# Kernel optimization log

Hardware: AMD Instinct MI355X
Metric: run time of the kernel (lower is better)

## Reference

```python
import jax, jax.numpy as jnp
import numpy as np
import math

B, C, D_FEAT, D_TASK, HID = 1024, 256, 512, 512, 32


def setup_inputs() -> dict:
    key = jax.random.key(0)
    ks = jax.random.split(key, 10)
    def xavier(k, shape, gain):
        fan_out, fan_in = shape
        a = gain * math.sqrt(6.0 / (fan_in + fan_out))
        return jax.random.uniform(k, shape, jnp.float32, -a, a)
    return {
        "Q": jax.random.normal(ks[0], (B, D_TASK), jnp.float32),
        "features": jax.random.normal(ks[1], (B, C, D_FEAT), jnp.float32),
        "Wk_w": xavier(ks[2], (D_TASK, D_FEAT), 0.1),
        "Wk_b": jnp.zeros((D_TASK,), jnp.float32),
        "Wv_w": xavier(ks[3], (D_TASK, D_FEAT), 0.1),
        "Wv_b": jnp.zeros((D_TASK,), jnp.float32),
        "g1_w": xavier(ks[4], (HID, D_TASK + 1), 1.0),
        "g1_b": jax.random.uniform(ks[5], (HID,), jnp.float32, -1.0, 1.0) / math.sqrt(D_TASK + 1),
        "g2_w": xavier(ks[6], (1, HID), 0.1),
        "g2_b": jnp.zeros((1,), jnp.float32),
    }


def reference(Q, features, Wk_w, Wk_b, Wv_w, Wv_b, g1_w, g1_b, g2_w, g2_b):
    # K, V projections: [B, C, d_task]
    K = jnp.einsum('bcf,tf->bct', features, Wk_w) + Wk_b
    V = jnp.einsum('bcf,tf->bct', features, Wv_w) + Wv_b
    # single-query cross-attention
    scores = jnp.einsum('bt,bct->bc', Q, K) / math.sqrt(D_TASK)  # [B, C]
    weights = jax.nn.softmax(scores, axis=-1)
    feat_read = jnp.einsum('bc,bct->bt', weights, V)  # [B, d_task]
    # gate from (Q, feature scale)
    feat_scale = jnp.mean(jnp.abs(features), axis=(1, 2), keepdims=False)[:, None]  # [B, 1]
    h = jnp.concatenate([Q, feat_scale], axis=-1)  # [B, d_task+1]
    h = jax.nn.gelu(h @ g1_w.T + g1_b, approximate=False)
    gate = jax.nn.sigmoid(h @ g2_w.T + g2_b)  # [B, 1]
    return gate * feat_read, gate
```

## Files before the change

### kernel.cpp

```cpp
#include <hip/hip_runtime.h>
#include <math.h>

constexpr int B = 1024, C = 256, DF = 512, DT = 512, HID = 32;

__global__ __launch_bounds__(256) void qproj_kernel(const float* __restrict__ Q,
                                                    const float* __restrict__ Wk,
                                                    float* __restrict__ qtil) {
    __shared__ __align__(16) float qs[4][DT];
    const int tid = threadIdx.x;
    const int b0 = blockIdx.x * 4;
#pragma unroll
    for (int bb = 0; bb < 4; bb++) {
        qs[bb][tid]       = Q[(b0 + bb) * DT + tid];
        qs[bb][tid + 256] = Q[(b0 + bb) * DT + tid + 256];
    }
    __syncthreads();
    const int f0 = tid * 2;
    float acc0[4] = {0.f, 0.f, 0.f, 0.f};
    float acc1[4] = {0.f, 0.f, 0.f, 0.f};
    for (int t4 = 0; t4 < DT; t4 += 4) {
        float q[4][4];
#pragma unroll
        for (int bb = 0; bb < 4; bb++) {
            float4 qv = *(const float4*)&qs[bb][t4];
            q[bb][0] = qv.x; q[bb][1] = qv.y; q[bb][2] = qv.z; q[bb][3] = qv.w;
        }
#pragma unroll
        for (int k = 0; k < 4; k++) {
            float2 w = *(const float2*)(Wk + (size_t)(t4 + k) * DF + f0);
#pragma unroll
            for (int bb = 0; bb < 4; bb++) {
                acc0[bb] += q[bb][k] * w.x;
                acc1[bb] += q[bb][k] * w.y;
            }
        }
    }
#pragma unroll
    for (int bb = 0; bb < 4; bb++) {
        float2 o; o.x = acc0[bb]; o.y = acc1[bb];
        *(float2*)(qtil + (size_t)(b0 + bb) * DF + f0) = o;
    }
}

__global__ __launch_bounds__(256) void main_kernel(
    const float* __restrict__ Q, const float* __restrict__ feat,
    const float* __restrict__ qtil,
    const float* __restrict__ Wv, const float* __restrict__ Wvb,
    const float* __restrict__ g1w, const float* __restrict__ g1b,
    const float* __restrict__ g2w, const float* __restrict__ g2b,
    float* __restrict__ out0, float* __restrict__ out1) {

    __shared__ __align__(16) float s_q[DF];
    __shared__ __align__(16) float s_Q[DT];
    __shared__ __align__(16) float s_part[4][DF];
    __shared__ __align__(16) float s_r[DF];
    __shared__ __align__(16) float s_out[DT];
    __shared__ float s_m[4], s_l[4], s_abs[4];
    __shared__ float s_hp[HID][8];
    __shared__ float s_h[HID];
    __shared__ float s_gate;

    const int tid  = threadIdx.x;
    const int lane = tid & 63;
    const int wv   = tid >> 6;
    const int b    = blockIdx.x;

    s_q[tid]       = qtil[b * DF + tid];
    s_q[tid + 256] = qtil[b * DF + tid + 256];
    s_Q[tid]       = Q[b * DT + tid];
    s_Q[tid + 256] = Q[b * DT + tid + 256];
    __syncthreads();

    float qreg[8];
    {
        float4 a0 = *(const float4*)&s_q[lane * 8];
        float4 a1 = *(const float4*)&s_q[lane * 8 + 4];
        qreg[0] = a0.x; qreg[1] = a0.y; qreg[2] = a0.z; qreg[3] = a0.w;
        qreg[4] = a1.x; qreg[5] = a1.y; qreg[6] = a1.z; qreg[7] = a1.w;
    }

    const float* fb = feat + (size_t)b * C * DF;
    float r[8] = {0.f, 0.f, 0.f, 0.f, 0.f, 0.f, 0.f, 0.f};
    float m = -INFINITY, l = 0.f, sabs = 0.f;
    const float rs = 0.044194173824159216f;

    for (int c = wv * 64; c < wv * 64 + 64; c += 2) {
        const float* row0 = fb + (size_t)c * DF + lane * 8;
        const float* row1 = row0 + DF;
        float4 x0a = *(const float4*)row0;
        float4 x0b = *(const float4*)(row0 + 4);
        float4 x1a = *(const float4*)row1;
        float4 x1b = *(const float4*)(row1 + 4);
        float v0[8] = {x0a.x, x0a.y, x0a.z, x0a.w, x0b.x, x0b.y, x0b.z, x0b.w};
        float v1[8] = {x1a.x, x1a.y, x1a.z, x1a.w, x1b.x, x1b.y, x1b.z, x1b.w};
        float dot0 = 0.f, dot1 = 0.f;
#pragma unroll
        for (int j = 0; j < 8; j++) {
            dot0 += v0[j] * qreg[j];
            dot1 += v1[j] * qreg[j];
            sabs += fabsf(v0[j]) + fabsf(v1[j]);
        }
#pragma unroll
        for (int off = 1; off < 64; off <<= 1) {
            dot0 += __shfl_xor(dot0, off, 64);
            dot1 += __shfl_xor(dot1, off, 64);
        }
        float s0 = dot0 * rs, s1 = dot1 * rs;
        float m2 = fmaxf(fmaxf(m, s0), s1);
        float a  = __expf(m - m2);
        float p0 = __expf(s0 - m2);
        float p1 = __expf(s1 - m2);
        l = l * a + p0 + p1;
#pragma unroll
        for (int j = 0; j < 8; j++) r[j] = r[j] * a + p0 * v0[j] + p1 * v1[j];
        m = m2;
    }
#pragma unroll
    for (int off = 1; off < 64; off <<= 1) sabs += __shfl_xor(sabs, off, 64);
    if (lane == 0) { s_m[wv] = m; s_l[wv] = l; s_abs[wv] = sabs; }
    __syncthreads();

    float M = fmaxf(fmaxf(s_m[0], s_m[1]), fmaxf(s_m[2], s_m[3]));
    float L = s_l[0] * __expf(s_m[0] - M) + s_l[1] * __expf(s_m[1] - M) +
              s_l[2] * __expf(s_m[2] - M) + s_l[3] * __expf(s_m[3] - M);
    float msc = __expf(m - M);
#pragma unroll
    for (int j = 0; j < 8; j++) s_part[wv][lane * 8 + j] = r[j] * msc;
    float fscale = (s_abs[0] + s_abs[1] + s_abs[2] + s_abs[3]) * (1.0f / (float)(C * DF));
    __syncthreads();

    float invL = 1.0f / L;
#pragma unroll
    for (int k = 0; k < 2; k++) {
        int f = tid + 256 * k;
        s_r[f] = (s_part[0][f] + s_part[1][f] + s_part[2][f] + s_part[3][f]) * invL;
    }

    {
        int i = tid >> 3, g = tid & 7;
        const float* row = g1w + (size_t)i * (DT + 1);
        float part = 0.f;
        for (int t = g * 64; t < g * 64 + 64; ++t) part += row[t] * s_Q[t];
        if (g == 0) part += row[DT] * fscale;
        s_hp[i][g] = part;
    }
    __syncthreads();
    if (tid < HID) {
        float x = g1b[tid];
#pragma unroll
        for (int g = 0; g < 8; ++g) x += s_hp[tid][g];
        s_h[tid] = 0.5f * x * (1.0f + erff(x * 0.70710678118654752f));
    }
    __syncthreads();
    if (tid == 0) {
        float z = g2b[0];
        for (int i = 0; i < HID; ++i) z += s_h[i] * g2w[i];
        float gate = 1.0f / (1.0f + __expf(-z));
        s_gate = gate;
        out1[b] = gate;
    }
    __syncthreads();

    float gate = s_gate;
    float rr[8];
    {
        float4 a0 = *(const float4*)&s_r[lane * 8];
        float4 a1 = *(const float4*)&s_r[lane * 8 + 4];
        rr[0] = a0.x; rr[1] = a0.y; rr[2] = a0.z; rr[3] = a0.w;
        rr[4] = a1.x; rr[5] = a1.y; rr[6] = a1.z; rr[7] = a1.w;
    }
    for (int t = wv * 128; t < wv * 128 + 128; t += 2) {
        const float* w0p = Wv + (size_t)t * DF + lane * 8;
        const float* w1p = w0p + DF;
        float4 w0a = *(const float4*)w0p;
        float4 w0b = *(const float4*)(w0p + 4);
        float4 w1a = *(const float4*)w1p;
        float4 w1b = *(const float4*)(w1p + 4);
        float dot0 = w0a.x * rr[0] + w0a.y * rr[1] + w0a.z * rr[2] + w0a.w * rr[3]
                   + w0b.x * rr[4] + w0b.y * rr[5] + w0b.z * rr[6] + w0b.w * rr[7];
        float dot1 = w1a.x * rr[0] + w1a.y * rr[1] + w1a.z * rr[2] + w1a.w * rr[3]
                   + w1b.x * rr[4] + w1b.y * rr[5] + w1b.z * rr[6] + w1b.w * rr[7];
#pragma unroll
        for (int off = 1; off < 64; off <<= 1) {
            dot0 += __shfl_xor(dot0, off, 64);
            dot1 += __shfl_xor(dot1, off, 64);
        }
        if (lane == 0) {
            s_out[t]     = gate * (dot0 + Wvb[t]);
            s_out[t + 1] = gate * (dot1 + Wvb[t + 1]);
        }
    }
    __syncthreads();
    float2 o;
    o.x = s_out[2 * tid];
    o.y = s_out[2 * tid + 1];
    *(float2*)(out0 + (size_t)b * DT + 2 * tid) = o;
}

extern "C" void kernel_launch(void* const* d_in, const int* in_sizes, int n_in,
                              void* d_out, int out_size, void* d_ws, size_t ws_size,
                              hipStream_t stream) {
    const float* Q    = (const float*)d_in[0];
    const float* feat = (const float*)d_in[1];
    const float* Wk   = (const float*)d_in[2];
    const float* Wv   = (const float*)d_in[4];
    const float* Wvb  = (const float*)d_in[5];
    const float* g1w  = (const float*)d_in[6];
    const float* g1b  = (const float*)d_in[7];
    const float* g2w  = (const float*)d_in[8];
    const float* g2b  = (const float*)d_in[9];
    float* out0 = (float*)d_out;
    float* out1 = out0 + (size_t)B * DT;
    float* qtil = (float*)d_ws;

    hipLaunchKernelGGL(qproj_kernel, dim3(B / 4), dim3(256), 0, stream, Q, Wk, qtil);
    hipLaunchKernelGGL(main_kernel, dim3(B), dim3(256), 0, stream,
                       Q, feat, qtil, Wv, Wvb, g1w, g1b, g2w, g2b, out0, out1);
}
```

Before: 790.8 us.

## Split V projection into separate kernel batching four rows per Wv pass

```diff
diff --git a/kernel.cpp b/kernel.cpp
--- a/kernel.cpp
+++ b/kernel.cpp
@@ -45,20 +45,16 @@
 __global__ __launch_bounds__(256) void main_kernel(
     const float* __restrict__ Q, const float* __restrict__ feat,
     const float* __restrict__ qtil,
-    const float* __restrict__ Wv, const float* __restrict__ Wvb,
     const float* __restrict__ g1w, const float* __restrict__ g1b,
     const float* __restrict__ g2w, const float* __restrict__ g2b,
-    float* __restrict__ out0, float* __restrict__ out1) {
+    float* __restrict__ rg, float* __restrict__ out1) {
 
     __shared__ __align__(16) float s_q[DF];
     __shared__ __align__(16) float s_Q[DT];
     __shared__ __align__(16) float s_part[4][DF];
-    __shared__ __align__(16) float s_r[DF];
-    __shared__ __align__(16) float s_out[DT];
     __shared__ float s_m[4], s_l[4], s_abs[4];
     __shared__ float s_hp[HID][8];
     __shared__ float s_h[HID];
-    __shared__ float s_gate;
 
     const int tid  = threadIdx.x;
     const int lane = tid & 63;
@@ -133,7 +129,8 @@
 #pragma unroll
     for (int k = 0; k < 2; k++) {
         int f = tid + 256 * k;
-        s_r[f] = (s_part[0][f] + s_part[1][f] + s_part[2][f] + s_part[3][f]) * invL;
+        float val = (s_part[0][f] + s_part[1][f] + s_part[2][f] + s_part[3][f]) * invL;
+        rg[(size_t)b * DF + f] = val;
     }
 
     {
@@ -155,46 +152,82 @@
     if (tid == 0) {
         float z = g2b[0];
         for (int i = 0; i < HID; ++i) z += s_h[i] * g2w[i];
-        float gate = 1.0f / (1.0f + __expf(-z));
-        s_gate = gate;
-        out1[b] = gate;
-    }
-    __syncthreads();
-
-    float gate = s_gate;
-    float rr[8];
+        out1[b] = 1.0f / (1.0f + __expf(-z));
+    }
+}
+
+__global__ __launch_bounds__(512) void vproj_kernel(
+    const float* __restrict__ rg, const float* __restrict__ gates,
+    const float* __restrict__ Wv, const float* __restrict__ Wvb,
+    float* __restrict__ out0) {
+
+    __shared__ __align__(16) float s_r4[4][DF];
+    __shared__ __align__(16) float s_o[4][DT];
+
+    const int tid  = threadIdx.x;
+    const int lane = tid & 63;
+    const int wv   = tid >> 6;
+    const int b0   = blockIdx.x * 4;
+
     {
-        float4 a0 = *(const float4*)&s_r[lane * 8];
-        float4 a1 = *(const float4*)&s_r[lane * 8 + 4];
-        rr[0] = a0.x; rr[1] = a0.y; rr[2] = a0.z; rr[3] = a0.w;
-        rr[4] = a1.x; rr[5] = a1.y; rr[6] = a1.z; rr[7] = a1.w;
-    }
-    for (int t = wv * 128; t < wv * 128 + 128; t += 2) {
+        const float* src = rg + (size_t)b0 * DF;
+        float* dst = &s_r4[0][0];
+#pragma unroll
+        for (int k = 0; k < 4; k++) dst[tid + 512 * k] = src[tid + 512 * k];
+    }
+    __syncthreads();
+
+    float rr[4][8];
+#pragma unroll
+    for (int bb = 0; bb < 4; bb++) {
+        float4 a0 = *(const float4*)&s_r4[bb][lane * 8];
+        float4 a1 = *(const float4*)&s_r4[bb][lane * 8 + 4];
+        rr[bb][0] = a0.x; rr[bb][1] = a0.y; rr[bb][2] = a0.z; rr[bb][3] = a0.w;
+        rr[bb][4] = a1.x; rr[bb][5] = a1.y; rr[bb][6] = a1.z; rr[bb][7] = a1.w;
+    }
+    float g4[4];
+#pragma unroll
+    for (int bb = 0; bb < 4; bb++) g4[bb] = gates[b0 + bb];
+
+    for (int t = wv * 64; t < wv * 64 + 64; t += 2) {
         const float* w0p = Wv + (size_t)t * DF + lane * 8;
         const float* w1p = w0p + DF;
         float4 w0a = *(const float4*)w0p;
         float4 w0b = *(const float4*)(w0p + 4);
         float4 w1a = *(const float4*)w1p;
         float4 w1b = *(const float4*)(w1p + 4);
-        float dot0 = w0a.x * rr[0] + w0a.y * rr[1] + w0a.z * rr[2] + w0a.w * rr[3]
-                   + w0b.x * rr[4] + w0b.y * rr[5] + w0b.z * rr[6] + w0b.w * rr[7];
-        float dot1 = w1a.x * rr[0] + w1a.y * rr[1] + w1a.z * rr[2] + w1a.w * rr[3]
-                   + w1b.x * rr[4] + w1b.y * rr[5] + w1b.z * rr[6] + w1b.w * rr[7];
+        float w0[8] = {w0a.x, w0a.y, w0a.z, w0a.w, w0b.x, w0b.y, w0b.z, w0b.w};
+        float w1[8] = {w1a.x, w1a.y, w1a.z, w1a.w, w1b.x, w1b.y, w1b.z, w1b.w};
+        float d0[4], d1[4];
+#pragma unroll
+        for (int bb = 0; bb < 4; bb++) {
+            float a = 0.f, c = 0.f;
+#pragma unroll
+            for (int j = 0; j < 8; j++) {
+                a += w0[j] * rr[bb][j];
+                c += w1[j] * rr[bb][j];
+            }
+            d0[bb] = a; d1[bb] = c;
+        }
 #pragma unroll
         for (int off = 1; off < 64; off <<= 1) {
-            dot0 += __shfl_xor(dot0, off, 64);
-            dot1 += __shfl_xor(dot1, off, 64);
+#pragma unroll
+            for (int bb = 0; bb < 4; bb++) {
+                d0[bb] += __shfl_xor(d0[bb], off, 64);
+                d1[bb] += __shfl_xor(d1[bb], off, 64);
+            }
         }
         if (lane == 0) {
-            s_out[t]     = gate * (dot0 + Wvb[t]);
-            s_out[t + 1] = gate * (dot1 + Wvb[t + 1]);
-        }
-    }
-    __syncthreads();
-    float2 o;
-    o.x = s_out[2 * tid];
-    o.y = s_out[2 * tid + 1];
-    *(float2*)(out0 + (size_t)b * DT + 2 * tid) = o;
+            float vb0 = Wvb[t], vb1 = Wvb[t + 1];
+#pragma unroll
+            for (int bb = 0; bb < 4; bb++) {
+                s_o[bb][t]     = g4[bb] * (d0[bb] + vb0);
+                s_o[bb][t + 1] = g4[bb] * (d1[bb] + vb1);
+            }
+        }
+    }
+    __syncthreads();
+    *(float4*)(out0 + (size_t)b0 * DT + 4 * tid) = *(const float4*)(&s_o[0][0] + 4 * tid);
 }
 
 extern "C" void kernel_launch(void* const* d_in, const int* in_sizes, int n_in,
@@ -212,8 +245,11 @@
     float* out0 = (float*)d_out;
     float* out1 = out0 + (size_t)B * DT;
     float* qtil = (float*)d_ws;
+    float* rg   = (float*)d_ws + (size_t)B * DF;
 
     hipLaunchKernelGGL(qproj_kernel, dim3(B / 4), dim3(256), 0, stream, Q, Wk, qtil);
     hipLaunchKernelGGL(main_kernel, dim3(B), dim3(256), 0, stream,
-                       Q, feat, qtil, Wv, Wvb, g1w, g1b, g2w, g2b, out0, out1);
-}
+                       Q, feat, qtil, g1w, g1b, g2w, g2b, rg, out1);
+    hipLaunchKernelGGL(vproj_kernel, dim3(B / 4), dim3(512), 0, stream,
+                       rg, out1, Wv, Wvb, out0);
+}
```

New measurement: 790.6 us. About the same (-0.0%).
